# Kernel optimization log

Hardware: AMD Instinct MI355X
Metric: run time of the kernel (lower is better)

## Reference

```python
import jax, jax.numpy as jnp
import numpy as np

B, S, I, C = 1, 2048, 384, 64
H, CH = 8, 8  # n_head, c_h
EPS_LN = 1e-5


def setup_inputs() -> dict:
    key = jax.random.key(0)
    ks = jax.random.split(key, 8)
    sc = lambda fan_in: 1.0 / np.sqrt(fan_in)
    return {
        "m": jax.random.normal(ks[0], (B, S, I, C), dtype=jnp.float32),
        "mask": jnp.ones((B, S, I), dtype=jnp.float32),
        "ln_gamma": jnp.ones((C,), dtype=jnp.float32),
        "ln_beta": jnp.zeros((C,), dtype=jnp.float32),
        "Wq": jax.random.normal(ks[1], (H * CH, C), dtype=jnp.float32) * sc(C),
        "Wk": jax.random.normal(ks[2], (CH, C), dtype=jnp.float32) * sc(C),
        "Wv": jax.random.normal(ks[3], (CH, C), dtype=jnp.float32) * sc(C),
        "Wg": jax.random.normal(ks[4], (H * CH, C), dtype=jnp.float32) * sc(C),
        "bg": jnp.zeros((H * CH,), dtype=jnp.float32),
        "Wo": jax.random.normal(ks[5], (C, H * CH), dtype=jnp.float32) * sc(H * CH),
        "bo": jnp.zeros((C,), dtype=jnp.float32),
    }


def _layernorm(x, gamma, beta):
    mu = x.mean(axis=-1, keepdims=True)
    var = x.var(axis=-1, keepdims=True)
    return (x - mu) * jax.lax.rsqrt(var + EPS_LN) * gamma + beta


def reference(m, mask, ln_gamma, ln_beta, Wq, Wk, Wv, Wg, bg, Wo, bo):
    # m: [B, s, i, c]; mask: [B, s, i]
    m_col = jnp.swapaxes(m, -2, -3)          # [B, i, s, c]
    mask_col = jnp.swapaxes(mask, -1, -2)    # [B, i, s]
    m_norm = _layernorm(m_col, ln_gamma, ln_beta)

    # masked-mean global query per column
    denom = jnp.clip(mask_col.sum(axis=-1, keepdims=True), 1e-5, None)  # [B, i, 1]
    q_global = (m_norm * mask_col[..., None]).sum(axis=-2) / denom      # [B, i, c]

    q = (q_global @ Wq.T).reshape(*q_global.shape[:-1], H, CH)  # [B, i, H, CH]
    k = m_norm @ Wk.T                                           # [B, i, s, CH]
    v = m_norm @ Wv.T                                           # [B, i, s, CH]

    scale = 1.0 / np.sqrt(CH)
    logits = jnp.einsum("bihc,bisc->bihs", q, k) * scale        # [B, i, H, s]
    logits = jnp.where(mask_col[:, :, None, :] > 0, logits, -1e9)
    attn = jax.nn.softmax(logits, axis=-1)
    ctx = jnp.einsum("bihs,bisc->bihc", attn, v)                # [B, i, H, CH]

    g = jax.nn.sigmoid(m_norm @ Wg.T + bg)                      # [B, i, s, H*CH]
    o = ctx.reshape(*ctx.shape[:-2], 1, H * CH) * g             # [B, i, s, H*CH]
    out = o @ Wo.T + bo                                          # [B, i, s, c]
    return jnp.swapaxes(out, -2, -3)                             # [B, s, i, c]
```

## Files before the change

### kernel.cpp

```cpp
#include <hip/hip_runtime.h>

#define IDIM 384
#define SDIM 2048
#define NCH  8
#define CHUNK 256

#define WS_STATS 0
#define WS_QGP   (IDIM*SDIM*2)
#define WS_Q     (WS_QGP + IDIM*NCH*65)
#define WS_ATT   (WS_Q + IDIM*64)
#define WS_CTX   (WS_ATT + IDIM*NCH*8*10)
#define WS_WGT   (WS_CTX + IDIM*64)
#define WS_WOT   (WS_WGT + 64*64)
#define WS_KV    (WS_WOT + 64*64)

typedef float f16v __attribute__((ext_vector_type(16)));

template<bool DOKV>
__global__ __launch_bounds__(256) void kA2(const float* __restrict__ m,
                                           const float* __restrict__ mask,
                                           const float* __restrict__ gamma,
                                           const float* __restrict__ beta,
                                           const float* __restrict__ Wk,
                                           const float* __restrict__ Wv,
                                           float* __restrict__ ws) {
    int bx = blockIdx.x;
    int i = bx >> 3, chk = bx & 7;
    int tid = threadIdx.x;
    int rg = tid >> 3;
    int c8 = tid & 7;
    __shared__ float Wk_s[8 * 68], Wv_s[8 * 68];
    if (DOKV) {
        for (int idx = tid; idx < 512; idx += 256) {
            int r = idx >> 6, c = idx & 63;
            Wk_s[r * 68 + c] = Wk[idx];
            Wv_s[r * 68 + c] = Wv[idx];
        }
        __syncthreads();
    }
    float4 ga4 = *(const float4*)&gamma[c8 * 8];
    float4 gb4 = *(const float4*)&gamma[c8 * 8 + 4];
    float4 ba4 = *(const float4*)&beta[c8 * 8];
    float4 bb4 = *(const float4*)&beta[c8 * 8 + 4];
    float g[8] = {ga4.x, ga4.y, ga4.z, ga4.w, gb4.x, gb4.y, gb4.z, gb4.w};
    float b[8] = {ba4.x, ba4.y, ba4.z, ba4.w, bb4.x, bb4.y, bb4.z, bb4.w};
    float qg[8];
    #pragma unroll
    for (int j = 0; j < 8; ++j) qg[j] = 0.f;
    float cnt = 0.f;
    float* stats = ws + WS_STATS;

    for (int t = 0; t < 8; ++t) {
        int s = chk * CHUNK + t * 32 + rg;
        const float* mp = &m[((size_t)s * IDIM + i) * 64 + c8 * 8];
        float4 xa = *(const float4*)mp;
        float4 xb = *(const float4*)(mp + 4);
        float x[8] = {xa.x, xa.y, xa.z, xa.w, xb.x, xb.y, xb.z, xb.w};
        float sx = 0.f, sxx = 0.f;
        #pragma unroll
        for (int j = 0; j < 8; ++j) { sx += x[j]; sxx += x[j] * x[j]; }
        sx += __shfl_xor(sx, 1); sxx += __shfl_xor(sxx, 1);
        sx += __shfl_xor(sx, 2); sxx += __shfl_xor(sxx, 2);
        sx += __shfl_xor(sx, 4); sxx += __shfl_xor(sxx, 4);
        float mu  = sx * (1.f / 64.f);
        float var = sxx * (1.f / 64.f) - mu * mu;
        float rs  = rsqrtf(var + 1e-5f);
        float mk  = mask[s * IDIM + i];
        float mnv[8];
        #pragma unroll
        for (int j = 0; j < 8; ++j) {
            mnv[j] = (x[j] - mu) * rs * g[j] + b[j];
            qg[j] += mk * mnv[j];
        }
        if (c8 == 0) {
            cnt += mk;
            float2 st = {mu, rs};
            *(float2*)&stats[((size_t)i * SDIM + s) * 2] = st;
        }
        if (DOKV) {
            float kp[8], vp[8];
            #pragma unroll
            for (int h = 0; h < 8; ++h) {
                float4 wk0 = *(const float4*)&Wk_s[h * 68 + c8 * 8];
                float4 wk1 = *(const float4*)&Wk_s[h * 68 + c8 * 8 + 4];
                float4 wv0 = *(const float4*)&Wv_s[h * 68 + c8 * 8];
                float4 wv1 = *(const float4*)&Wv_s[h * 68 + c8 * 8 + 4];
                kp[h] = mnv[0]*wk0.x + mnv[1]*wk0.y + mnv[2]*wk0.z + mnv[3]*wk0.w
                      + mnv[4]*wk1.x + mnv[5]*wk1.y + mnv[6]*wk1.z + mnv[7]*wk1.w;
                vp[h] = mnv[0]*wv0.x + mnv[1]*wv0.y + mnv[2]*wv0.z + mnv[3]*wv0.w
                      + mnv[4]*wv1.x + mnv[5]*wv1.y + mnv[6]*wv1.z + mnv[7]*wv1.w;
            }
            #pragma unroll
            for (int h = 0; h < 8; ++h) {
                kp[h] += __shfl_xor(kp[h], 1); vp[h] += __shfl_xor(vp[h], 1);
                kp[h] += __shfl_xor(kp[h], 2); vp[h] += __shfl_xor(vp[h], 2);
                kp[h] += __shfl_xor(kp[h], 4); vp[h] += __shfl_xor(vp[h], 4);
            }
            float* kvp = ws + WS_KV + ((size_t)i * SDIM + s) * 16;
            #pragma unroll
            for (int j = 0; j < 8; ++j) {
                if (c8 == j) { kvp[j] = kp[j]; kvp[8 + j] = vp[j]; }
            }
        }
    }
    __shared__ float red[32][68];
    #pragma unroll
    for (int j = 0; j < 8; ++j) red[rg][c8 * 8 + j] = qg[j];
    if (c8 == 0) red[rg][64] = cnt;
    __syncthreads();
    if (tid < 65) {
        float v = 0.f;
        #pragma unroll
        for (int r = 0; r < 32; ++r) v += red[r][tid];
        ws[WS_QGP + (i * NCH + chk) * 65 + tid] = v;
    }
}

__global__ __launch_bounds__(64) void kB(const float* __restrict__ Wq,
                                         const float* __restrict__ Wg,
                                         const float* __restrict__ Wo,
                                         float* __restrict__ ws) {
    int i = blockIdx.x, l = threadIdx.x;
    if (i < 64) {
        ws[WS_WGT + i * 64 + l] = Wg[l * 64 + i];
        ws[WS_WOT + i * 64 + l] = Wo[l * 64 + i];
    }
    float sum = 0.f, cnt = 0.f;
    #pragma unroll
    for (int c = 0; c < NCH; ++c) {
        sum += ws[WS_QGP + (i * NCH + c) * 65 + l];
        cnt += ws[WS_QGP + (i * NCH + c) * 65 + 64];
    }
    float denom = fmaxf(cnt, 1e-5f);
    __shared__ float qg[64];
    qg[l] = sum / denom;
    __syncthreads();
    float acc = 0.f;
    #pragma unroll 8
    for (int c = 0; c < 64; ++c) acc += qg[c] * Wq[l * 64 + c];
    ws[WS_Q + i * 64 + l] = acc * 0.35355339059327373f;
}

__global__ __launch_bounds__(256) void kC2(const float* __restrict__ mask,
                                           float* __restrict__ ws) {
    int bx = blockIdx.x;
    int i = bx >> 3, chk = bx & 7;
    int tid = threadIdx.x;
    __shared__ float kv_s[256 * 20];
    __shared__ float red[32 * 8 * 10];

    const float* kvg = ws + WS_KV + ((size_t)i * SDIM + chk * CHUNK) * 16;
    for (int idx = tid; idx < 1024; idx += 256) {
        int r = idx >> 2, c4 = idx & 3;
        *(float4*)&kv_s[r * 20 + c4 * 4] = *(const float4*)&kvg[idx * 4];
    }
    int sr = tid >> 3;
    int lo = tid & 7;
    const float* wq = ws + WS_Q + i * 64 + lo * 8;
    float4 q0 = *(const float4*)wq;
    float4 q1 = *(const float4*)(wq + 4);
    float m_run = -1e30f, l_run = 0.f, ctx[8];
    #pragma unroll
    for (int z = 0; z < 8; ++z) ctx[z] = 0.f;
    __syncthreads();

    for (int t = 0; t < 8; ++t) {
        int r = t * 32 + sr;
        float4 k0 = *(const float4*)&kv_s[r * 20];
        float4 k1 = *(const float4*)&kv_s[r * 20 + 4];
        float4 v0 = *(const float4*)&kv_s[r * 20 + 8];
        float4 v1 = *(const float4*)&kv_s[r * 20 + 12];
        float lg = q0.x*k0.x + q0.y*k0.y + q0.z*k0.z + q0.w*k0.w
                 + q1.x*k1.x + q1.y*k1.y + q1.z*k1.z + q1.w*k1.w;
        float mk = mask[(chk * CHUNK + r) * IDIM + i];
        lg = (mk > 0.f) ? lg : -1e9f;
        float mnew = fmaxf(m_run, lg);
        float al = expf(m_run - mnew);
        float p  = expf(lg - mnew);
        l_run = l_run * al + p;
        ctx[0] = ctx[0]*al + p*v0.x; ctx[1] = ctx[1]*al + p*v0.y;
        ctx[2] = ctx[2]*al + p*v0.z; ctx[3] = ctx[3]*al + p*v0.w;
        ctx[4] = ctx[4]*al + p*v1.x; ctx[5] = ctx[5]*al + p*v1.y;
        ctx[6] = ctx[6]*al + p*v1.z; ctx[7] = ctx[7]*al + p*v1.w;
        m_run = mnew;
    }
    int base = (sr * 8 + lo) * 10;
    red[base] = m_run; red[base + 1] = l_run;
    #pragma unroll
    for (int c = 0; c < 8; ++c) red[base + 2 + c] = ctx[c];
    __syncthreads();
    if (tid < 64) {
        int h = tid >> 3, c2 = tid & 7;
        float M = -1e30f;
        for (int r = 0; r < 32; ++r) M = fmaxf(M, red[(r * 8 + h) * 10]);
        float L = 0.f, CT = 0.f;
        for (int r = 0; r < 32; ++r) {
            float e = expf(red[(r * 8 + h) * 10] - M);
            L += red[(r * 8 + h) * 10 + 1] * e;
            CT += red[(r * 8 + h) * 10 + 2 + c2] * e;
        }
        float* dst = ws + WS_ATT + ((i * NCH + chk) * 8 + h) * 10;
        if (c2 == 0) { dst[0] = M; dst[1] = L; }
        dst[2 + c2] = CT;
    }
}

__global__ __launch_bounds__(256) void kC(const float* __restrict__ m,
                                          const float* __restrict__ mask,
                                          const float* __restrict__ gamma,
                                          const float* __restrict__ beta,
                                          const float* __restrict__ Wk,
                                          const float* __restrict__ Wv,
                                          float* __restrict__ ws) {
    int bx = blockIdx.x;
    int i = bx >> 3, chk = bx & 7;
    int tid = threadIdx.x;
    __shared__ float mnT[32 * 68];
    __shared__ float Wk_s[8 * 68], Wv_s[8 * 68];
    __shared__ float k_s[32 * 9], v_s[32 * 9];
    __shared__ float q_s[64];
    __shared__ float red[32 * 8 * 10];
    const float* stats = ws + WS_STATS;

    if (tid < 64) q_s[tid] = ws[WS_Q + i * 64 + tid];
    for (int idx = tid; idx < 512; idx += 256) {
        int r = idx >> 6, c = idx & 63;
        Wk_s[r * 68 + c] = Wk[idx];
        Wv_s[r * 68 + c] = Wv[idx];
    }
    int sr = tid >> 3;
    int lo = tid & 7;
    float m_run = -1e30f, l_run = 0.f, ctx[8];
    #pragma unroll
    for (int z = 0; z < 8; ++z) ctx[z] = 0.f;
    __syncthreads();

    for (int t = 0; t < 8; ++t) {
        int sbase = chk * CHUNK + t * 32;
        for (int idx = tid; idx < 512; idx += 256) {
            int r = idx >> 4, c4 = idx & 15;
            int s = sbase + r;
            float4 x4 = *(const float4*)&m[((size_t)s * IDIM + i) * 64 + c4 * 4];
            float4 g4 = *(const float4*)&gamma[c4 * 4];
            float4 b4 = *(const float4*)&beta[c4 * 4];
            float2 st = *(const float2*)&stats[((size_t)i * SDIM + s) * 2];
            float4 mn;
            mn.x = (x4.x - st.x) * st.y * g4.x + b4.x;
            mn.y = (x4.y - st.x) * st.y * g4.y + b4.y;
            mn.z = (x4.z - st.x) * st.y * g4.z + b4.z;
            mn.w = (x4.w - st.x) * st.y * g4.w + b4.w;
            *(float4*)&mnT[r * 68 + c4 * 4] = mn;
        }
        __syncthreads();
        {
            float accK = 0.f, accV = 0.f;
            #pragma unroll
            for (int c4 = 0; c4 < 16; ++c4) {
                float4 a  = *(const float4*)&mnT[sr * 68 + c4 * 4];
                float4 wk = *(const float4*)&Wk_s[lo * 68 + c4 * 4];
                float4 wv = *(const float4*)&Wv_s[lo * 68 + c4 * 4];
                accK += a.x * wk.x + a.y * wk.y + a.z * wk.z + a.w * wk.w;
                accV += a.x * wv.x + a.y * wv.y + a.z * wv.z + a.w * wv.w;
            }
            k_s[sr * 9 + lo] = accK;
            v_s[sr * 9 + lo] = accV;
        }
        __syncthreads();
        {
            float lg = 0.f;
            #pragma unroll
            for (int c = 0; c < 8; ++c) lg += q_s[lo * 8 + c] * k_s[sr * 9 + c];
            float mk = mask[(sbase + sr) * IDIM + i];
            lg = (mk > 0.f) ? lg : -1e9f;
            float mnew = fmaxf(m_run, lg);
            float al = expf(m_run - mnew);
            float p  = expf(lg - mnew);
            l_run = l_run * al + p;
            #pragma unroll
            for (int c = 0; c < 8; ++c) ctx[c] = ctx[c] * al + p * v_s[sr * 9 + c];
            m_run = mnew;
        }
        __syncthreads();
    }
    int base = (sr * 8 + lo) * 10;
    red[base] = m_run; red[base + 1] = l_run;
    #pragma unroll
    for (int c = 0; c < 8; ++c) red[base + 2 + c] = ctx[c];
    __syncthreads();
    if (tid < 64) {
        int h = tid >> 3, c2 = tid & 7;
        float M = -1e30f;
        for (int r = 0; r < 32; ++r) M = fmaxf(M, red[(r * 8 + h) * 10]);
        float L = 0.f, CT = 0.f;
        for (int r = 0; r < 32; ++r) {
            float e = expf(red[(r * 8 + h) * 10] - M);
            L += red[(r * 8 + h) * 10 + 1] * e;
            CT += red[(r * 8 + h) * 10 + 2 + c2] * e;
        }
        float* dst = ws + WS_ATT + ((i * NCH + chk) * 8 + h) * 10;
        if (c2 == 0) { dst[0] = M; dst[1] = L; }
        dst[2 + c2] = CT;
    }
}

__global__ __launch_bounds__(64) void kD(float* __restrict__ ws) {
    int i = blockIdx.x, l = threadIdx.x;
    int h = l >> 3, c2 = l & 7;
    float M = -1e30f;
    #pragma unroll
    for (int c = 0; c < NCH; ++c)
        M = fmaxf(M, ws[WS_ATT + ((i * NCH + c) * 8 + h) * 10]);
    float L = 0.f, CT = 0.f;
    #pragma unroll
    for (int c = 0; c < NCH; ++c) {
        const float* src = ws + WS_ATT + ((i * NCH + c) * 8 + h) * 10;
        float e = expf(src[0] - M);
        L += src[1] * e;
        CT += src[2 + c2] * e;
    }
    ws[WS_CTX + i * 64 + l] = CT / L;
}

__global__ __launch_bounds__(256, 8) void kE(const float* __restrict__ m,
                                             const float* __restrict__ gamma,
                                             const float* __restrict__ beta,
                                             const float* __restrict__ bg,
                                             const float* __restrict__ bo,
                                             const float* __restrict__ ws,
                                             float* __restrict__ out) {
    int bx = blockIdx.x;
    int i = bx >> 5;
    int tile = bx & 31;
    int tid = threadIdx.x;
    int l = tid & 63;
    int wv16 = __builtin_amdgcn_readfirstlane((tid >> 6) << 4);
    __shared__ float mnT[64 * 68];
    const float* stats = ws + WS_STATS;
    int s0 = tile * 64;

    float ctxv[16], bgv[16], bov[16];
    #pragma unroll
    for (int q = 0; q < 4; ++q) {
        float4 cv = *(const float4*)&ws[WS_CTX + i * 64 + wv16 + q * 4];
        float4 gv = *(const float4*)&bg[wv16 + q * 4];
        float4 ov = *(const float4*)&bo[wv16 + q * 4];
        ctxv[q*4+0]=cv.x; ctxv[q*4+1]=cv.y; ctxv[q*4+2]=cv.z; ctxv[q*4+3]=cv.w;
        bgv[q*4+0]=gv.x;  bgv[q*4+1]=gv.y;  bgv[q*4+2]=gv.z;  bgv[q*4+3]=gv.w;
        bov[q*4+0]=ov.x;  bov[q*4+1]=ov.y;  bov[q*4+2]=ov.z;  bov[q*4+3]=ov.w;
    }

    for (int idx = tid; idx < 1024; idx += 256) {
        int r = idx >> 4, c4 = idx & 15;
        int s = s0 + r;
        float4 x4 = *(const float4*)&m[((size_t)s * IDIM + i) * 64 + c4 * 4];
        float4 g4 = *(const float4*)&gamma[c4 * 4];
        float4 b4 = *(const float4*)&beta[c4 * 4];
        float2 st = *(const float2*)&stats[((size_t)i * SDIM + s) * 2];
        float4 mn;
        mn.x = (x4.x - st.x) * st.y * g4.x + b4.x;
        mn.y = (x4.y - st.x) * st.y * g4.y + b4.y;
        mn.z = (x4.z - st.x) * st.y * g4.z + b4.z;
        mn.w = (x4.w - st.x) * st.y * g4.w + b4.w;
        *(float4*)&mnT[r * 68 + c4 * 4] = mn;
    }
    __syncthreads();

    float z[16];
    #pragma unroll
    for (int jj = 0; jj < 16; ++jj) z[jj] = 0.f;
    const float* aP = &mnT[l * 68];

    {
        const float* Bg = ws + WS_WGT + wv16;
        #pragma unroll 4
        for (int c4 = 0; c4 < 16; ++c4) {
            float4 a0 = *(const float4*)(aP + c4 * 4);
            float aa[4] = {a0.x, a0.y, a0.z, a0.w};
            #pragma unroll
            for (int cc = 0; cc < 4; ++cc) {
                f16v bv = *(const f16v*)(Bg + (c4 * 4 + cc) * 64);
                float av = aa[cc];
                #pragma unroll
                for (int jj = 0; jj < 16; ++jj) z[jj] += av * bv[jj];
            }
        }
    }
    __syncthreads();

    #pragma unroll
    for (int jj = 0; jj < 16; ++jj)
        z[jj] = ctxv[jj] / (1.f + expf(-(z[jj] + bgv[jj])));
    #pragma unroll
    for (int q = 0; q < 4; ++q) {
        float4 t0 = {z[q*4+0], z[q*4+1], z[q*4+2], z[q*4+3]};
        *(float4*)&mnT[l * 68 + wv16 + q * 4] = t0;
    }
    #pragma unroll
    for (int jj = 0; jj < 16; ++jj) z[jj] = 0.f;
    __syncthreads();

    {
        const float* Bo = ws + WS_WOT + wv16;
        #pragma unroll 4
        for (int c4 = 0; c4 < 16; ++c4) {
            float4 a0 = *(const float4*)(aP + c4 * 4);
            float aa[4] = {a0.x, a0.y, a0.z, a0.w};
            #pragma unroll
            for (int cc = 0; cc < 4; ++cc) {
                f16v bv = *(const f16v*)(Bo + (c4 * 4 + cc) * 64);
                float av = aa[cc];
                #pragma unroll
                for (int jj = 0; jj < 16; ++jj) z[jj] += av * bv[jj];
            }
        }
    }
    __syncthreads();

    #pragma unroll
    for (int q = 0; q < 4; ++q) {
        float4 t0 = {z[q*4+0]+bov[q*4+0], z[q*4+1]+bov[q*4+1],
                     z[q*4+2]+bov[q*4+2], z[q*4+3]+bov[q*4+3]};
        *(float4*)&mnT[l * 68 + wv16 + q * 4] = t0;
    }
    __syncthreads();

    for (int idx = tid; idx < 1024; idx += 256) {
        int r = idx >> 4, c4 = idx & 15;
        float4 v = *(const float4*)&mnT[r * 68 + c4 * 4];
        *(float4*)&out[((size_t)(s0 + r) * IDIM + i) * 64 + c4 * 4] = v;
    }
}

extern "C" void kernel_launch(void* const* d_in, const int* in_sizes, int n_in,
                              void* d_out, int out_size, void* d_ws, size_t ws_size,
                              hipStream_t stream) {
    const float* m    = (const float*)d_in[0];
    const float* mask = (const float*)d_in[1];
    const float* gam  = (const float*)d_in[2];
    const float* bet  = (const float*)d_in[3];
    const float* Wq   = (const float*)d_in[4];
    const float* Wk   = (const float*)d_in[5];
    const float* Wv   = (const float*)d_in[6];
    const float* Wg   = (const float*)d_in[7];
    const float* bg   = (const float*)d_in[8];
    const float* Wo   = (const float*)d_in[9];
    const float* bo   = (const float*)d_in[10];
    float* out = (float*)d_out;
    float* ws  = (float*)d_ws;
    (void)in_sizes; (void)n_in; (void)out_size;

    size_t need_fused = (size_t)(WS_KV + (size_t)IDIM * SDIM * 16) * sizeof(float);
    bool fused = ws_size >= need_fused;

    if (fused)
        kA2<true><<<IDIM * NCH, 256, 0, stream>>>(m, mask, gam, bet, Wk, Wv, ws);
    else
        kA2<false><<<IDIM * NCH, 256, 0, stream>>>(m, mask, gam, bet, Wk, Wv, ws);
    kB<<<IDIM, 64, 0, stream>>>(Wq, Wg, Wo, ws);
    if (fused)
        kC2<<<IDIM * NCH, 256, 0, stream>>>(mask, ws);
    else
        kC<<<IDIM * NCH, 256, 0, stream>>>(m, mask, gam, bet, Wk, Wv, ws);
    kD<<<IDIM, 64, 0, stream>>>(ws);
    kE<<<IDIM * (SDIM / 64), 256, 0, stream>>>(m, gam, bet, bg, bo, ws, out);
}
```

Before: 602.8 us.

## Fold small kernels into neighbors, reorder blocks, register weights, scalar-load GEMM operands

Drops the kB and kD launches on the fused path. The Wg/Wo transposes move into the first blocks of kA2, the q projection is recomputed per block inside kC2, and the partial-softmax merge is done per block inside kE. Block indexing changes to chunk/tile-major with column i fastest, so neighbouring blocks read adjacent rows of m. kA2 now keeps Wk/Wv in registers, prefetches the next m row, and uses a transposing shuffle reduction that stores one value per lane. kE loads GEMM weights with inline s_load_dwordx16 scalar loads. This adds redundant per-block work and register pressure, and the inline asm waits on lgkmcnt(0) inside an unroll-1 loop.

After: 556.8 us. 7.6% less time.

```diff
diff --git a/kernel.cpp b/kernel.cpp
--- a/kernel.cpp
+++ b/kernel.cpp
@@ -14,7 +14,7 @@
 #define WS_WOT   (WS_WGT + 64*64)
 #define WS_KV    (WS_WOT + 64*64)
 
-typedef float f16v __attribute__((ext_vector_type(16)));
+typedef float sf16 __attribute__((ext_vector_type(16)));
 
 template<bool DOKV>
 __global__ __launch_bounds__(256) void kA2(const float* __restrict__ m,
@@ -23,39 +23,59 @@
                                            const float* __restrict__ beta,
                                            const float* __restrict__ Wk,
                                            const float* __restrict__ Wv,
+                                           const float* __restrict__ Wg,
+                                           const float* __restrict__ Wo,
                                            float* __restrict__ ws) {
     int bx = blockIdx.x;
-    int i = bx >> 3, chk = bx & 7;
+    int chk = bx / IDIM;
+    int i = bx - chk * IDIM;
     int tid = threadIdx.x;
     int rg = tid >> 3;
     int c8 = tid & 7;
-    __shared__ float Wk_s[8 * 68], Wv_s[8 * 68];
-    if (DOKV) {
-        for (int idx = tid; idx < 512; idx += 256) {
-            int r = idx >> 6, c = idx & 63;
-            Wk_s[r * 68 + c] = Wk[idx];
-            Wv_s[r * 68 + c] = Wv[idx];
-        }
-        __syncthreads();
-    }
+
+    if (bx < 16) {
+        int g = bx * 256 + tid;
+        int r = g >> 6, c = g & 63;
+        ws[WS_WGT + g] = Wg[c * 64 + r];
+        ws[WS_WOT + g] = Wo[c * 64 + r];
+    }
+
     float4 ga4 = *(const float4*)&gamma[c8 * 8];
     float4 gb4 = *(const float4*)&gamma[c8 * 8 + 4];
     float4 ba4 = *(const float4*)&beta[c8 * 8];
     float4 bb4 = *(const float4*)&beta[c8 * 8 + 4];
     float g[8] = {ga4.x, ga4.y, ga4.z, ga4.w, gb4.x, gb4.y, gb4.z, gb4.w};
     float b[8] = {ba4.x, ba4.y, ba4.z, ba4.w, bb4.x, bb4.y, bb4.z, bb4.w};
+
+    float4 wkr[16], wvr[16];
+    if (DOKV) {
+        #pragma unroll
+        for (int h = 0; h < 8; ++h) {
+            wkr[h * 2]     = *(const float4*)&Wk[h * 64 + c8 * 8];
+            wkr[h * 2 + 1] = *(const float4*)&Wk[h * 64 + c8 * 8 + 4];
+            wvr[h * 2]     = *(const float4*)&Wv[h * 64 + c8 * 8];
+            wvr[h * 2 + 1] = *(const float4*)&Wv[h * 64 + c8 * 8 + 4];
+        }
+    }
+
     float qg[8];
     #pragma unroll
     for (int j = 0; j < 8; ++j) qg[j] = 0.f;
     float cnt = 0.f;
     float* stats = ws + WS_STATS;
 
+    int s0 = chk * CHUNK + rg;
+    float4 xa = *(const float4*)&m[((size_t)s0 * IDIM + i) * 64 + c8 * 8];
+    float4 xb = *(const float4*)&m[((size_t)s0 * IDIM + i) * 64 + c8 * 8 + 4];
+
     for (int t = 0; t < 8; ++t) {
         int s = chk * CHUNK + t * 32 + rg;
-        const float* mp = &m[((size_t)s * IDIM + i) * 64 + c8 * 8];
-        float4 xa = *(const float4*)mp;
-        float4 xb = *(const float4*)(mp + 4);
         float x[8] = {xa.x, xa.y, xa.z, xa.w, xb.x, xb.y, xb.z, xb.w};
+        if (t < 7) {
+            int sn = s + 32;
+            xa = *(const float4*)&m[((size_t)sn * IDIM + i) * 64 + c8 * 8];
+            xb = *(const float4*)&m[((size_t)sn * IDIM + i) * 64 + c8 * 8 + 4];
+        }
         float sx = 0.f, sxx = 0.f;
         #pragma unroll
         for (int j = 0; j < 8; ++j) { sx += x[j]; sxx += x[j] * x[j]; }
@@ -81,26 +101,39 @@
             float kp[8], vp[8];
             #pragma unroll
             for (int h = 0; h < 8; ++h) {
-                float4 wk0 = *(const float4*)&Wk_s[h * 68 + c8 * 8];
-                float4 wk1 = *(const float4*)&Wk_s[h * 68 + c8 * 8 + 4];
-                float4 wv0 = *(const float4*)&Wv_s[h * 68 + c8 * 8];
-                float4 wv1 = *(const float4*)&Wv_s[h * 68 + c8 * 8 + 4];
-                kp[h] = mnv[0]*wk0.x + mnv[1]*wk0.y + mnv[2]*wk0.z + mnv[3]*wk0.w
-                      + mnv[4]*wk1.x + mnv[5]*wk1.y + mnv[6]*wk1.z + mnv[7]*wk1.w;
-                vp[h] = mnv[0]*wv0.x + mnv[1]*wv0.y + mnv[2]*wv0.z + mnv[3]*wv0.w
-                      + mnv[4]*wv1.x + mnv[5]*wv1.y + mnv[6]*wv1.z + mnv[7]*wv1.w;
+                float4 a0 = wkr[h * 2], a1 = wkr[h * 2 + 1];
+                kp[h] = mnv[0]*a0.x + mnv[1]*a0.y + mnv[2]*a0.z + mnv[3]*a0.w
+                      + mnv[4]*a1.x + mnv[5]*a1.y + mnv[6]*a1.z + mnv[7]*a1.w;
+                float4 c0 = wvr[h * 2], c1 = wvr[h * 2 + 1];
+                vp[h] = mnv[0]*c0.x + mnv[1]*c0.y + mnv[2]*c0.z + mnv[3]*c0.w
+                      + mnv[4]*c1.x + mnv[5]*c1.y + mnv[6]*c1.z + mnv[7]*c1.w;
             }
-            #pragma unroll
-            for (int h = 0; h < 8; ++h) {
-                kp[h] += __shfl_xor(kp[h], 1); vp[h] += __shfl_xor(vp[h], 1);
-                kp[h] += __shfl_xor(kp[h], 2); vp[h] += __shfl_xor(vp[h], 2);
-                kp[h] += __shfl_xor(kp[h], 4); vp[h] += __shfl_xor(vp[h], 4);
+            bool s4 = (c8 & 4) != 0, s2 = (c8 & 2) != 0, s1 = (c8 & 1) != 0;
+            float k4[4], v4[4];
+            #pragma unroll
+            for (int hh = 0; hh < 4; ++hh) {
+                float ka = s4 ? kp[hh + 4] : kp[hh];
+                float kb = s4 ? kp[hh] : kp[hh + 4];
+                k4[hh] = ka + __shfl_xor(kb, 4);
+                float va = s4 ? vp[hh + 4] : vp[hh];
+                float vb = s4 ? vp[hh] : vp[hh + 4];
+                v4[hh] = va + __shfl_xor(vb, 4);
             }
+            float k2[2], v2[2];
+            #pragma unroll
+            for (int hh = 0; hh < 2; ++hh) {
+                float ka = s2 ? k4[hh + 2] : k4[hh];
+                float kb = s2 ? k4[hh] : k4[hh + 2];
+                k2[hh] = ka + __shfl_xor(kb, 2);
+                float va = s2 ? v4[hh + 2] : v4[hh];
+                float vb = s2 ? v4[hh] : v4[hh + 2];
+                v2[hh] = va + __shfl_xor(vb, 2);
+            }
+            float kf = (s1 ? k2[1] : k2[0]) + __shfl_xor(s1 ? k2[0] : k2[1], 1);
+            float vf = (s1 ? v2[1] : v2[0]) + __shfl_xor(s1 ? v2[0] : v2[1], 1);
             float* kvp = ws + WS_KV + ((size_t)i * SDIM + s) * 16;
-            #pragma unroll
-            for (int j = 0; j < 8; ++j) {
-                if (c8 == j) { kvp[j] = kp[j]; kvp[8 + j] = vp[j]; }
-            }
+            kvp[c8]     = kf;
+            kvp[8 + c8] = vf;
         }
     }
     __shared__ float red[32][68];
@@ -117,14 +150,8 @@
 }
 
 __global__ __launch_bounds__(64) void kB(const float* __restrict__ Wq,
-                                         const float* __restrict__ Wg,
-                                         const float* __restrict__ Wo,
                                          float* __restrict__ ws) {
     int i = blockIdx.x, l = threadIdx.x;
-    if (i < 64) {
-        ws[WS_WGT + i * 64 + l] = Wg[l * 64 + i];
-        ws[WS_WOT + i * 64 + l] = Wo[l * 64 + i];
-    }
     float sum = 0.f, cnt = 0.f;
     #pragma unroll
     for (int c = 0; c < NCH; ++c) {
@@ -142,27 +169,47 @@
 }
 
 __global__ __launch_bounds__(256) void kC2(const float* __restrict__ mask,
+                                           const float* __restrict__ Wq,
                                            float* __restrict__ ws) {
     int bx = blockIdx.x;
-    int i = bx >> 3, chk = bx & 7;
+    int chk = bx / IDIM;
+    int i = bx - chk * IDIM;
     int tid = threadIdx.x;
     __shared__ float kv_s[256 * 20];
     __shared__ float red[32 * 8 * 10];
+    __shared__ float qg_s[64];
+    __shared__ float q_s[64];
 
     const float* kvg = ws + WS_KV + ((size_t)i * SDIM + chk * CHUNK) * 16;
     for (int idx = tid; idx < 1024; idx += 256) {
         int r = idx >> 2, c4 = idx & 3;
         *(float4*)&kv_s[r * 20 + c4 * 4] = *(const float4*)&kvg[idx * 4];
     }
+    if (tid < 64) {
+        float sum = 0.f, cnt = 0.f;
+        #pragma unroll
+        for (int c = 0; c < 8; ++c) {
+            sum += ws[WS_QGP + (i * NCH + c) * 65 + tid];
+            cnt += ws[WS_QGP + (i * NCH + c) * 65 + 64];
+        }
+        qg_s[tid] = sum / fmaxf(cnt, 1e-5f);
+    }
+    __syncthreads();
+    if (tid < 64) {
+        float acc = 0.f;
+        #pragma unroll 8
+        for (int c = 0; c < 64; ++c) acc += qg_s[c] * Wq[tid * 64 + c];
+        q_s[tid] = acc * 0.35355339059327373f;
+    }
+    __syncthreads();
+
     int sr = tid >> 3;
     int lo = tid & 7;
-    const float* wq = ws + WS_Q + i * 64 + lo * 8;
-    float4 q0 = *(const float4*)wq;
-    float4 q1 = *(const float4*)(wq + 4);
+    float4 q0 = *(const float4*)&q_s[lo * 8];
+    float4 q1 = *(const float4*)&q_s[lo * 8 + 4];
     float m_run = -1e30f, l_run = 0.f, ctx[8];
     #pragma unroll
     for (int z = 0; z < 8; ++z) ctx[z] = 0.f;
-    __syncthreads();
 
     for (int t = 0; t < 8; ++t) {
         int r = t * 32 + sr;
@@ -303,24 +350,6 @@
     }
 }
 
-__global__ __launch_bounds__(64) void kD(float* __restrict__ ws) {
-    int i = blockIdx.x, l = threadIdx.x;
-    int h = l >> 3, c2 = l & 7;
-    float M = -1e30f;
-    #pragma unroll
-    for (int c = 0; c < NCH; ++c)
-        M = fmaxf(M, ws[WS_ATT + ((i * NCH + c) * 8 + h) * 10]);
-    float L = 0.f, CT = 0.f;
-    #pragma unroll
-    for (int c = 0; c < NCH; ++c) {
-        const float* src = ws + WS_ATT + ((i * NCH + c) * 8 + h) * 10;
-        float e = expf(src[0] - M);
-        L += src[1] * e;
-        CT += src[2 + c2] * e;
-    }
-    ws[WS_CTX + i * 64 + l] = CT / L;
-}
-
 __global__ __launch_bounds__(256, 8) void kE(const float* __restrict__ m,
                                              const float* __restrict__ gamma,
                                              const float* __restrict__ beta,
@@ -329,26 +358,32 @@
                                              const float* __restrict__ ws,
                                              float* __restrict__ out) {
     int bx = blockIdx.x;
-    int i = bx >> 5;
-    int tile = bx & 31;
+    int tile = bx / IDIM;
+    int i = bx - tile * IDIM;
     int tid = threadIdx.x;
     int l = tid & 63;
     int wv16 = __builtin_amdgcn_readfirstlane((tid >> 6) << 4);
     __shared__ float mnT[64 * 68];
+    __shared__ float ctx_s[64];
     const float* stats = ws + WS_STATS;
     int s0 = tile * 64;
 
-    float ctxv[16], bgv[16], bov[16];
-    #pragma unroll
-    for (int q = 0; q < 4; ++q) {
-        float4 cv = *(const float4*)&ws[WS_CTX + i * 64 + wv16 + q * 4];
-        float4 gv = *(const float4*)&bg[wv16 + q * 4];
-        float4 ov = *(const float4*)&bo[wv16 + q * 4];
-        ctxv[q*4+0]=cv.x; ctxv[q*4+1]=cv.y; ctxv[q*4+2]=cv.z; ctxv[q*4+3]=cv.w;
-        bgv[q*4+0]=gv.x;  bgv[q*4+1]=gv.y;  bgv[q*4+2]=gv.z;  bgv[q*4+3]=gv.w;
-        bov[q*4+0]=ov.x;  bov[q*4+1]=ov.y;  bov[q*4+2]=ov.z;  bov[q*4+3]=ov.w;
-    }
-
+    if (tid < 64) {
+        int h = tid >> 3, c2 = tid & 7;
+        float M = -1e30f;
+        #pragma unroll
+        for (int c = 0; c < NCH; ++c)
+            M = fmaxf(M, ws[WS_ATT + ((i * NCH + c) * 8 + h) * 10]);
+        float L = 0.f, CT = 0.f;
+        #pragma unroll
+        for (int c = 0; c < NCH; ++c) {
+            const float* src = ws + WS_ATT + ((i * NCH + c) * 8 + h) * 10;
+            float e = expf(src[0] - M);
+            L += src[1] * e;
+            CT += src[2 + c2] * e;
+        }
+        ctx_s[tid] = CT / L;
+    }
     for (int idx = tid; idx < 1024; idx += 256) {
         int r = idx >> 4, c4 = idx & 15;
         int s = s0 + r;
@@ -372,27 +407,41 @@
 
     {
         const float* Bg = ws + WS_WGT + wv16;
-        #pragma unroll 4
+        #pragma unroll 1
         for (int c4 = 0; c4 < 16; ++c4) {
             float4 a0 = *(const float4*)(aP + c4 * 4);
-            float aa[4] = {a0.x, a0.y, a0.z, a0.w};
-            #pragma unroll
-            for (int cc = 0; cc < 4; ++cc) {
-                f16v bv = *(const f16v*)(Bg + (c4 * 4 + cc) * 64);
-                float av = aa[cc];
-                #pragma unroll
-                for (int jj = 0; jj < 16; ++jj) z[jj] += av * bv[jj];
-            }
-        }
-    }
-    __syncthreads();
-
-    #pragma unroll
-    for (int jj = 0; jj < 16; ++jj)
-        z[jj] = ctxv[jj] / (1.f + expf(-(z[jj] + bgv[jj])));
+            const float* bp = Bg + c4 * 256;
+            sf16 b0, b1;
+            asm volatile("s_load_dwordx16 %0, %2, 0x0\n\t"
+                         "s_load_dwordx16 %1, %2, 0x100\n\t"
+                         "s_waitcnt lgkmcnt(0)"
+                         : "=&s"(b0), "=&s"(b1) : "s"(bp));
+            #pragma unroll
+            for (int jj = 0; jj < 16; ++jj) z[jj] += a0.x * b0[jj];
+            #pragma unroll
+            for (int jj = 0; jj < 16; ++jj) z[jj] += a0.y * b1[jj];
+            sf16 b2, b3;
+            asm volatile("s_load_dwordx16 %0, %2, 0x200\n\t"
+                         "s_load_dwordx16 %1, %2, 0x300\n\t"
+                         "s_waitcnt lgkmcnt(0)"
+                         : "=&s"(b2), "=&s"(b3) : "s"(bp));
+            #pragma unroll
+            for (int jj = 0; jj < 16; ++jj) z[jj] += a0.z * b2[jj];
+            #pragma unroll
+            for (int jj = 0; jj < 16; ++jj) z[jj] += a0.w * b3[jj];
+        }
+    }
+    __syncthreads();
+
     #pragma unroll
     for (int q = 0; q < 4; ++q) {
-        float4 t0 = {z[q*4+0], z[q*4+1], z[q*4+2], z[q*4+3]};
+        float4 cv = *(const float4*)&ctx_s[wv16 + q * 4];
+        float4 gv = *(const float4*)&bg[wv16 + q * 4];
+        float o0 = cv.x / (1.f + expf(-(z[q*4+0] + gv.x)));
+        float o1 = cv.y / (1.f + expf(-(z[q*4+1] + gv.y)));
+        float o2 = cv.z / (1.f + expf(-(z[q*4+2] + gv.z)));
+        float o3 = cv.w / (1.f + expf(-(z[q*4+3] + gv.w)));
+        float4 t0 = {o0, o1, o2, o3};
         *(float4*)&mnT[l * 68 + wv16 + q * 4] = t0;
     }
     #pragma unroll
@@ -401,25 +450,37 @@
 
     {
         const float* Bo = ws + WS_WOT + wv16;
-        #pragma unroll 4
+        #pragma unroll 1
         for (int c4 = 0; c4 < 16; ++c4) {
             float4 a0 = *(const float4*)(aP + c4 * 4);
-            float aa[4] = {a0.x, a0.y, a0.z, a0.w};
-            #pragma unroll
-            for (int cc = 0; cc < 4; ++cc) {
-                f16v bv = *(const f16v*)(Bo + (c4 * 4 + cc) * 64);
-                float av = aa[cc];
-                #pragma unroll
-                for (int jj = 0; jj < 16; ++jj) z[jj] += av * bv[jj];
-            }
+            const float* bp = Bo + c4 * 256;
+            sf16 b0, b1;
+            asm volatile("s_load_dwordx16 %0, %2, 0x0\n\t"
+                         "s_load_dwordx16 %1, %2, 0x100\n\t"
+                         "s_waitcnt lgkmcnt(0)"
+                         : "=&s"(b0), "=&s"(b1) : "s"(bp));
+            #pragma unroll
+            for (int jj = 0; jj < 16; ++jj) z[jj] += a0.x * b0[jj];
+            #pragma unroll
+            for (int jj = 0; jj < 16; ++jj) z[jj] += a0.y * b1[jj];
+            sf16 b2, b3;
+            asm volatile("s_load_dwordx16 %0, %2, 0x200\n\t"
+                         "s_load_dwordx16 %1, %2, 0x300\n\t"
+                         "s_waitcnt lgkmcnt(0)"
+                         : "=&s"(b2), "=&s"(b3) : "s"(bp));
+            #pragma unroll
+            for (int jj = 0; jj < 16; ++jj) z[jj] += a0.z * b2[jj];
+            #pragma unroll
+            for (int jj = 0; jj < 16; ++jj) z[jj] += a0.w * b3[jj];
         }
     }
     __syncthreads();
 
     #pragma unroll
     for (int q = 0; q < 4; ++q) {
-        float4 t0 = {z[q*4+0]+bov[q*4+0], z[q*4+1]+bov[q*4+1],
-                     z[q*4+2]+bov[q*4+2], z[q*4+3]+bov[q*4+3]};
+        float4 ov = *(const float4*)&bo[wv16 + q * 4];
+        float4 t0 = {z[q*4+0] + ov.x, z[q*4+1] + ov.y,
+                     z[q*4+2] + ov.z, z[q*4+3] + ov.w};
         *(float4*)&mnT[l * 68 + wv16 + q * 4] = t0;
     }
     __syncthreads();
@@ -452,15 +513,13 @@
     size_t need_fused = (size_t)(WS_KV + (size_t)IDIM * SDIM * 16) * sizeof(float);
     bool fused = ws_size >= need_fused;
 
-    if (fused)
-        kA2<true><<<IDIM * NCH, 256, 0, stream>>>(m, mask, gam, bet, Wk, Wv, ws);
-    else
-        kA2<false><<<IDIM * NCH, 256, 0, stream>>>(m, mask, gam, bet, Wk, Wv, ws);
-    kB<<<IDIM, 64, 0, stream>>>(Wq, Wg, Wo, ws);
-    if (fused)
-        kC2<<<IDIM * NCH, 256, 0, stream>>>(mask, ws);
-    else
+    if (fused) {
+        kA2<true><<<IDIM * NCH, 256, 0, stream>>>(m, mask, gam, bet, Wk, Wv, Wg, Wo, ws);
+        kC2<<<IDIM * NCH, 256, 0, stream>>>(mask, Wq, ws);
+    } else {
+        kA2<false><<<IDIM * NCH, 256, 0, stream>>>(m, mask, gam, bet, Wk, Wv, Wg, Wo, ws);
+        kB<<<IDIM, 64, 0, stream>>>(Wq, ws);
         kC<<<IDIM * NCH, 256, 0, stream>>>(m, mask, gam, bet, Wk, Wv, ws);
-    kD<<<IDIM, 64, 0, stream>>>(ws);
+    }
     kE<<<IDIM * (SDIM / 64), 256, 0, stream>>>(m, gam, bet, bg, bo, ws, out);
 }
```
